# Kernel optimization log

Hardware: AMD Instinct MI355X
Metric: run time of the kernel (lower is better)

## Reference

```python
import jax, jax.numpy as jnp
import numpy as np

N = 8192
D = 256


def setup_inputs() -> dict:
    key = jax.random.key(0)
    ks = jax.random.split(key, 10)
    s = 1.0 / np.sqrt(D)
    inp = {
        "embeddings": jax.random.normal(ks[0], (N, D), dtype=jnp.float32),
        "adjacency": jax.random.randint(ks[1], (N, N), 0, 2, dtype=jnp.int32),
        "Wq": jax.random.uniform(ks[2], (D, D), jnp.float32, -s, s),
        "bq": jax.random.uniform(ks[3], (D,), jnp.float32, -s, s),
        "Wk": jax.random.uniform(ks[4], (D, D), jnp.float32, -s, s),
        "bk": jax.random.uniform(ks[5], (D,), jnp.float32, -s, s),
        "Wv": jax.random.uniform(ks[6], (D, D), jnp.float32, -s, s),
        "bv": jax.random.uniform(ks[7], (D,), jnp.float32, -s, s),
        "Wo": jax.random.uniform(ks[8], (D, D), jnp.float32, -s, s),
        "bo": jax.random.uniform(ks[9], (D,), jnp.float32, -s, s),
    }
    return inp


def reference(embeddings, adjacency, Wq, bq, Wk, bk, Wv, bv, Wo, bo):
    # Q/K/V projections (torch Linear: x @ W.T + b)
    Q = embeddings @ Wq.T + bq            # [N, D]
    K = embeddings @ Wk.T + bk            # [N, D]
    V = embeddings @ Wv.T + bv            # [N, D]
    scale = 1.0 / jnp.sqrt(jnp.asarray(D, dtype=embeddings.dtype))
    scores = (Q @ K.T) * scale            # [N, N]
    scores = jnp.where(adjacency == 0, jnp.asarray(-1e9, scores.dtype), scores)
    attn = jax.nn.softmax(scores, axis=-1)  # dropout is identity in eval mode
    context = attn @ V                    # [N, D]
    return context @ Wo.T + bo
```

## Files before the change

kernel.cpp:

```cpp
#include <hip/hip_runtime.h>
#include <hip/hip_bf16.h>


#define LOG2E 1.44269504088896340736f
#define MASKVAL -3.0e38f
#define MINIT   -1.0e38f

using f32x4 = __attribute__((ext_vector_type(4))) float;
using s16x8 = __attribute__((ext_vector_type(8))) short;
using s16x4 = __attribute__((ext_vector_type(4))) short;

__device__ __forceinline__ void gl_lds16(void* l, const void* g) {
  __builtin_amdgcn_global_load_lds(
      (const __attribute__((address_space(1))) void*)g,
      (__attribute__((address_space(3))) void*)l, 16, 0, 0);
}

__device__ __forceinline__ short f2bf(float x) {
  union { float f; unsigned u; } v; v.f = x;
  unsigned r = v.u + 0x7fffu + ((v.u >> 16) & 1u);
  return (short)(r >> 16);
}

__device__ __forceinline__ s16x8 cvt_frag(f32x4 a, f32x4 b) {
  s16x8 r;
  r[0]=f2bf(a[0]); r[1]=f2bf(a[1]); r[2]=f2bf(a[2]); r[3]=f2bf(a[3]);
  r[4]=f2bf(b[0]); r[5]=f2bf(b[1]); r[6]=f2bf(b[2]); r[7]=f2bf(b[3]);
  return r;
}

__device__ __forceinline__ f32x4 mfma16(s16x8 a, s16x8 b, f32x4 c) {
  return __builtin_amdgcn_mfma_f32_16x16x32_bf16(a, b, c, 0, 0, 0);
}

__global__ __launch_bounds__(256, 2)
void qkv_kernel(const float* __restrict__ E,
                const float* __restrict__ Wq, const float* __restrict__ bq,
                const float* __restrict__ Wk, const float* __restrict__ bk,
                const float* __restrict__ Wv, const float* __restrict__ bv,
                unsigned short* __restrict__ Qb, unsigned short* __restrict__ Kb,
                unsigned short* __restrict__ VT)
{
  const int tid = threadIdx.x, lane = tid & 63, w = tid >> 6;
  const int wr = w >> 1, wc = w & 1;
  const int l15 = lane & 15, lhi = lane >> 4;
  const int m0 = blockIdx.x * 64 + wr * 32;
  const int n0 = blockIdx.y * 64 + wc * 32;

  s16x8 af[2][8];
#pragma unroll
  for (int m = 0; m < 2; ++m) {
    const float* ap = E + (size_t)(m0 + m * 16 + l15) * 256 + lhi * 8;
#pragma unroll
    for (int ks = 0; ks < 8; ++ks) {
      f32x4 lo = *(const f32x4*)(ap + ks * 32);
      f32x4 hi = *(const f32x4*)(ap + ks * 32 + 4);
      af[m][ks] = cvt_frag(lo, hi);
    }
  }

  const float* Ws[3] = {Wq, Wk, Wv};
  f32x4 acc[3][2][2] = {};
#pragma unroll
  for (int mtx = 0; mtx < 3; ++mtx)
#pragma unroll
    for (int n = 0; n < 2; ++n) {
      const float* bp = Ws[mtx] + (size_t)(n0 + n * 16 + l15) * 256 + lhi * 8;
#pragma unroll
      for (int ks = 0; ks < 8; ++ks) {
        f32x4 lo = *(const f32x4*)(bp + ks * 32);
        f32x4 hi = *(const f32x4*)(bp + ks * 32 + 4);
        s16x8 bf = cvt_frag(lo, hi);
#pragma unroll
        for (int m = 0; m < 2; ++m)
          acc[mtx][m][n] = mfma16(af[m][ks], bf, acc[mtx][m][n]);
      }
    }

#pragma unroll
  for (int n = 0; n < 2; ++n) {
    int col = n0 + n * 16 + l15;
    float bvq = bq[col], bvk = bk[col], bvv = bv[col];
#pragma unroll
    for (int m = 0; m < 2; ++m) {
      int rbase = m0 + m * 16 + lhi * 4;
#pragma unroll
      for (int r = 0; r < 4; ++r) {
        Qb[(size_t)(rbase + r) * 256 + col] = (unsigned short)f2bf((acc[0][m][n][r] + bvq) * 0.0625f);
        Kb[(size_t)(rbase + r) * 256 + col] = (unsigned short)f2bf(acc[1][m][n][r] + bvk);
      }
      s16x4 pk;
#pragma unroll
      for (int r = 0; r < 4; ++r) pk[r] = f2bf(acc[2][m][n][r] + bvv);
      *(s16x4*)(VT + (size_t)col * 8192 + rbase) = pk;
    }
  }
}

__global__ __launch_bounds__(256, 2)
void projo_kernel(const unsigned short* __restrict__ CX, const float* __restrict__ Wo,
                  const float* __restrict__ bo, float* __restrict__ outp)
{
  const int tid = threadIdx.x, lane = tid & 63, w = tid >> 6;
  const int wr = w >> 1, wc = w & 1;
  const int l15 = lane & 15, lhi = lane >> 4;
  const int m0 = blockIdx.x * 64 + wr * 32;
  const int n0 = blockIdx.y * 64 + wc * 32;

  s16x8 af[2][8];
#pragma unroll
  for (int m = 0; m < 2; ++m) {
    const unsigned short* ap = CX + (size_t)(m0 + m * 16 + l15) * 256 + lhi * 8;
#pragma unroll
    for (int ks = 0; ks < 8; ++ks) af[m][ks] = *(const s16x8*)(ap + ks * 32);
  }

  f32x4 acc[2][2] = {};
#pragma unroll
  for (int n = 0; n < 2; ++n) {
    const float* bp = Wo + (size_t)(n0 + n * 16 + l15) * 256 + lhi * 8;
#pragma unroll
    for (int ks = 0; ks < 8; ++ks) {
      f32x4 lo = *(const f32x4*)(bp + ks * 32);
      f32x4 hi = *(const f32x4*)(bp + ks * 32 + 4);
      s16x8 bf = cvt_frag(lo, hi);
#pragma unroll
      for (int m = 0; m < 2; ++m)
        acc[m][n] = mfma16(af[m][ks], bf, acc[m][n]);
    }
  }

#pragma unroll
  for (int n = 0; n < 2; ++n) {
    int col = n0 + n * 16 + l15;
    float bv = bo[col];
#pragma unroll
    for (int m = 0; m < 2; ++m) {
      int rbase = m0 + m * 16 + lhi * 4;
#pragma unroll
      for (int r = 0; r < 4; ++r)
        outp[(size_t)(rbase + r) * 256 + col] = acc[m][n][r] + bv;
    }
  }
}

template<int SPLIT, bool DIRECT, bool PACC_BF16>
__global__ __launch_bounds__(512, 2)
void attn_kernel(const unsigned short* __restrict__ Qb, const char* __restrict__ Kb,
                 const char* __restrict__ VbT, const int* __restrict__ adj,
                 void* __restrict__ pacc, float* __restrict__ pm,
                 float* __restrict__ pl, unsigned short* __restrict__ CX)
{
  __shared__ __align__(16) char ldsK[2][16384];
  __shared__ __align__(16) char ldsV[2][16384];
  __shared__ __align__(16) char ldsP[8][2048];
  const int tid = threadIdx.x, lane = tid & 63, w = tid >> 6;
  const int l15 = lane & 15, lhi = lane >> 4;
  const int qt = blockIdx.x / SPLIT, sp = blockIdx.x % SPLIT;
  const int q0 = qt * 256 + w * 32;
  char* myP = ldsP[w];
  const int kv_begin = sp * (8192 / SPLIT);
  const int NT = 8192 / SPLIT / 32;

  s16x8 qf[2][8];
#pragma unroll
  for (int f = 0; f < 2; ++f) {
    const unsigned short* qp = Qb + (size_t)(q0 + f * 16 + l15) * 256 + lhi * 8;
#pragma unroll
    for (int ks = 0; ks < 8; ++ks) qf[f][ks] = *(const s16x8*)(qp + ks * 32);
  }

  f32x4 ctx[2][16] = {};
  float m_run[2][4], l_run[2][4];
#pragma unroll
  for (int f = 0; f < 2; ++f)
#pragma unroll
    for (int r = 0; r < 4; ++r) { m_run[f][r] = MINIT; l_run[f][r] = 0.f; }

  auto STAGE = [&](int buf, int tt) {
    const int kv0 = kv_begin + tt * 32;
    const char* kg = Kb + (size_t)kv0 * 512;
#pragma unroll
    for (int i = 0; i < 2; ++i) {
      int o = tid * 16 + i * 8192;
      int row = o >> 9, inrow = o & 511;
      gl_lds16(&ldsK[buf][o], kg + row * 512 + (inrow ^ ((row & 7) << 4)));
    }
#pragma unroll
    for (int i = 0; i < 2; ++i) {
      int o = tid * 16 + i * 8192;
      int row = o >> 6, inrow = o & 63;
      gl_lds16(&ldsV[buf][o], VbT + (size_t)row * 16384 + (size_t)kv0 * 2 + (inrow ^ ((row & 3) << 4)));
    }
  };

  STAGE(0, 0);
  __syncthreads();

  const int* abase = adj + (size_t)(q0 + (lane >> 5)) * 8192 + (lane & 31);

  for (int t = 0; t < NT; ++t) {
    const int cur = t & 1;
    const int kv0 = kv_begin + t * 32;

    int av[16];
    {
      const int* ap = abase + kv0;
#pragma unroll
      for (int j = 0; j < 16; ++j) av[j] = ap[(size_t)j * 2 * 8192];
    }
    if (t + 1 < NT) STAGE(cur ^ 1, t + 1);

    f32x4 sacc[2][2] = {};
    __builtin_amdgcn_s_setprio(1);
#pragma unroll
    for (int ks = 0; ks < 8; ++ks)
#pragma unroll
      for (int cg = 0; cg < 2; ++cg) {
        int row = cg * 16 + l15;
        s16x8 kf = *(const s16x8*)(&ldsK[cur][row * 512 + ((ks * 64 + lhi * 16) ^ ((row & 7) << 4))]);
        sacc[0][cg] = mfma16(qf[0][ks], kf, sacc[0][cg]);
        sacc[1][cg] = mfma16(qf[1][ks], kf, sacc[1][cg]);
      }
    __builtin_amdgcn_s_setprio(0);

    unsigned bmv[2][4] = {};
#pragma unroll
    for (int j = 0; j < 16; ++j) {
      unsigned long long b = __ballot(av[j] != 0);
      unsigned lo = (unsigned)b, hi = (unsigned)(b >> 32);
      const int row0 = 2 * j;
      const int f = row0 >> 4, g = (row0 >> 2) & 3, r = row0 & 3;
      bmv[f][r]     = (lhi == g) ? lo : bmv[f][r];
      bmv[f][r + 1] = (lhi == g) ? hi : bmv[f][r + 1];
    }

#pragma unroll
    for (int f = 0; f < 2; ++f)
#pragma unroll
      for (int r = 0; r < 4; ++r) {
        unsigned ms = bmv[f][r] >> l15;
#pragma unroll
        for (int cg = 0; cg < 2; ++cg)
          if (!((ms >> (cg * 16)) & 1u)) sacc[f][cg][r] = MASKVAL;
      }

    float tmax[2][4];
#pragma unroll
    for (int f = 0; f < 2; ++f)
#pragma unroll
      for (int r = 0; r < 4; ++r)
        tmax[f][r] = fmaxf(sacc[f][0][r], sacc[f][1][r]);
#pragma unroll
    for (int mk = 1; mk <= 8; mk <<= 1)
#pragma unroll
      for (int f = 0; f < 2; ++f)
#pragma unroll
        for (int r = 0; r < 4; ++r)
          tmax[f][r] = fmaxf(tmax[f][r], __shfl_xor(tmax[f][r], mk, 64));

    float need = MASKVAL;
#pragma unroll
    for (int f = 0; f < 2; ++f)
#pragma unroll
      for (int r = 0; r < 4; ++r)
        need = fmaxf(need, tmax[f][r] - m_run[f][r]);
    if (!__all(need <= 8.0f)) {
#pragma unroll
      for (int f = 0; f < 2; ++f) {
        f32x4 fv;
#pragma unroll
        for (int r = 0; r < 4; ++r) {
          float mnew = fmaxf(m_run[f][r], tmax[f][r]);
          float fs = __builtin_amdgcn_exp2f((m_run[f][r] - mnew) * LOG2E);
          m_run[f][r] = mnew; l_run[f][r] *= fs; fv[r] = fs;
        }
#pragma unroll
        for (int dm = 0; dm < 16; ++dm) ctx[f][dm] *= fv;
      }
    }

#pragma unroll
    for (int f = 0; f < 2; ++f)
#pragma unroll
      for (int cg = 0; cg < 2; ++cg)
#pragma unroll
        for (int r = 0; r < 4; ++r) {
          float p = __builtin_amdgcn_exp2f((sacc[f][cg][r] - m_run[f][r]) * LOG2E);
          l_run[f][r] += p;
          int row = f * 16 + lhi * 4 + r;
          int cb = (cg * 16 + l15) * 2;
          *(short*)(myP + row * 64 + (cb ^ ((row & 3) << 4))) = f2bf(p);
        }

    __builtin_amdgcn_s_setprio(1);
    s16x8 pf[2];
#pragma unroll
    for (int f = 0; f < 2; ++f) {
      int prow = f * 16 + l15;
      pf[f] = *(const s16x8*)(myP + prow * 64 + ((lhi * 16) ^ ((prow & 3) << 4)));
    }
#pragma unroll
    for (int dm = 0; dm < 16; ++dm) {
      int vrow = dm * 16 + l15;
      s16x8 vf = *(const s16x8*)(&ldsV[cur][vrow * 64 + ((lhi * 16) ^ ((vrow & 3) << 4))]);
      ctx[0][dm] = mfma16(pf[0], vf, ctx[0][dm]);
      ctx[1][dm] = mfma16(pf[1], vf, ctx[1][dm]);
    }
    __builtin_amdgcn_s_setprio(0);

    __syncthreads();
  }

#pragma unroll
  for (int mk = 1; mk <= 8; mk <<= 1)
#pragma unroll
    for (int f = 0; f < 2; ++f)
#pragma unroll
      for (int r = 0; r < 4; ++r)
        l_run[f][r] += __shfl_xor(l_run[f][r], mk, 64);

  if (DIRECT) {
#pragma unroll
    for (int f = 0; f < 2; ++f)
#pragma unroll
      for (int r = 0; r < 4; ++r) {
        float inv = 1.0f / l_run[f][r];
        size_t rowb = (size_t)(q0 + f * 16 + lhi * 4 + r) * 256 + l15;
#pragma unroll
        for (int dm = 0; dm < 16; ++dm)
          CX[rowb + dm * 16] = (unsigned short)f2bf(ctx[f][dm][r] * inv);
      }
  } else {
#pragma unroll
    for (int f = 0; f < 2; ++f)
#pragma unroll
      for (int r = 0; r < 4; ++r) {
        size_t rowb = (size_t)sp * 8192 * 256 +
                      (size_t)(q0 + f * 16 + lhi * 4 + r) * 256 + l15;
        if (PACC_BF16) {
#pragma unroll
          for (int dm = 0; dm < 16; ++dm)
            ((unsigned short*)pacc)[rowb + dm * 16] = (unsigned short)f2bf(ctx[f][dm][r]);
        } else {
#pragma unroll
          for (int dm = 0; dm < 16; ++dm)
            ((float*)pacc)[rowb + dm * 16] = ctx[f][dm][r];
        }
      }
    if (l15 == 0) {
#pragma unroll
      for (int f = 0; f < 2; ++f)
#pragma unroll
        for (int r = 0; r < 4; ++r) {
          pm[(size_t)sp * 8192 + q0 + f * 16 + lhi * 4 + r] = m_run[f][r];
          pl[(size_t)sp * 8192 + q0 + f * 16 + lhi * 4 + r] = l_run[f][r];
        }
    }
  }
}

template<bool PACC_BF16>
__global__ __launch_bounds__(256)
void combine_kernel(const void* __restrict__ pacc, const float* __restrict__ pm,
                    const float* __restrict__ pl, unsigned short* __restrict__ cx)
{
  const int row = blockIdx.x;
  const int d = threadIdx.x;
  float M = MINIT;
#pragma unroll
  for (int s = 0; s < 8; ++s) M = fmaxf(M, pm[s * 8192 + row]);
  float L = 0.f, v = 0.f;
#pragma unroll
  for (int s = 0; s < 8; ++s) {
    float ws = __builtin_amdgcn_exp2f((pm[s * 8192 + row] - M) * LOG2E);
    L += ws * pl[s * 8192 + row];
    size_t idx = (size_t)s * 8192 * 256 + (size_t)row * 256 + d;
    float pv;
    if (PACC_BF16) {
      union { unsigned u; float f; } c; c.u = (unsigned)((const unsigned short*)pacc)[idx] << 16;
      pv = c.f;
    } else {
      pv = ((const float*)pacc)[idx];
    }
    v += ws * pv;
  }
  cx[(size_t)row * 256 + d] = (unsigned short)f2bf(v / L);
}

extern "C" void kernel_launch(void* const* d_in, const int* in_sizes, int n_in,
                              void* d_out, int out_size, void* d_ws, size_t ws_size,
                              hipStream_t stream)
{
  const float* E  = (const float*)d_in[0];
  const int*  adj = (const int*)d_in[1];
  const float* Wq = (const float*)d_in[2];
  const float* bq = (const float*)d_in[3];
  const float* Wk = (const float*)d_in[4];
  const float* bk = (const float*)d_in[5];
  const float* Wv = (const float*)d_in[6];
  const float* bv = (const float*)d_in[7];
  const float* Wo = (const float*)d_in[8];
  const float* bo = (const float*)d_in[9];

  char* ws = (char*)d_ws;
  unsigned short* Qb = (unsigned short*)(ws);
  unsigned short* Kb = (unsigned short*)(ws + ((size_t)4 << 20));
  unsigned short* VT = (unsigned short*)(ws + ((size_t)8 << 20));
  unsigned short* CX = (unsigned short*)(ws + ((size_t)12 << 20));
  char* pacc = ws + ((size_t)16 << 20);

  hipLaunchKernelGGL(qkv_kernel, dim3(128, 4), dim3(256), 0, stream,
                     E, Wq, bq, Wk, bk, Wv, bv, Qb, Kb, VT);

  const size_t PACC_F32_BYTES  = (size_t)8 * 8192 * 256 * 4;
  const size_t PACC_BF16_BYTES = (size_t)8 * 8192 * 256 * 2;
  const size_t PMPL = (size_t)8 * 8192 * 4;
  const size_t NEED_F32  = ((size_t)16 << 20) + PACC_F32_BYTES + 2 * PMPL;
  const size_t NEED_BF16 = ((size_t)16 << 20) + PACC_BF16_BYTES + 2 * PMPL;

  if (ws_size >= NEED_F32) {
    float* pm = (float*)(pacc + PACC_F32_BYTES);
    float* pl = pm + 8 * 8192;
    hipLaunchKernelGGL((attn_kernel<8, false, false>), dim3(256), dim3(512), 0, stream,
                       Qb, (const char*)Kb, (const char*)VT, adj, pacc, pm, pl, CX);
    hipLaunchKernelGGL((combine_kernel<false>), dim3(8192), dim3(256), 0, stream, pacc, pm, pl, CX);
  } else if (ws_size >= NEED_BF16) {
    float* pm = (float*)(pacc + PACC_BF16_BYTES);
    float* pl = pm + 8 * 8192;
    hipLaunchKernelGGL((attn_kernel<8, false, true>), dim3(256), dim3(512), 0, stream,
                       Qb, (const char*)Kb, (const char*)VT, adj, pacc, pm, pl, CX);
    hipLaunchKernelGGL((combine_kernel<true>), dim3(8192), dim3(256), 0, stream, pacc, pm, pl, CX);
  } else {
    float* pm = (float*)pacc; float* pl = pm + 8192;
    hipLaunchKernelGGL((attn_kernel<1, true, false>), dim3(32), dim3(512), 0, stream,
                       Qb, (const char*)Kb, (const char*)VT, adj, pacc, pm, pl, CX);
  }
  hipLaunchKernelGGL(projo_kernel, dim3(128, 4), dim3(256), 0, stream, CX, Wo, bo, (float*)d_out);
}
```

Baseline: 618.5 us.

## Load K and V fragments directly from global memory instead of LDS staging

Removes the double-buffered LDS staging of K and V tiles and the per-tile block barrier, so each wave loads its MFMA operands straight from global memory (relying on L2/L1 caching). Blocks shrink from 8 waves to 4, with twice as many blocks launched. This drops barrier stalls and LDS traffic, but each wave now issues redundant global loads of the same K/V data, and the gathers are strided (especially V rows 16 KB apart), which adds latency and cache pressure.

After: 704.9 us. +14.0%, slower.

```diff
diff --git a/kernel.cpp b/kernel.cpp
--- a/kernel.cpp
+++ b/kernel.cpp
@@ -9,12 +9,6 @@
 using f32x4 = __attribute__((ext_vector_type(4))) float;
 using s16x8 = __attribute__((ext_vector_type(8))) short;
 using s16x4 = __attribute__((ext_vector_type(4))) short;
-
-__device__ __forceinline__ void gl_lds16(void* l, const void* g) {
-  __builtin_amdgcn_global_load_lds(
-      (const __attribute__((address_space(1))) void*)g,
-      (__attribute__((address_space(3))) void*)l, 16, 0, 0);
-}
 
 __device__ __forceinline__ short f2bf(float x) {
   union { float f; unsigned u; } v; v.f = x;
@@ -145,19 +139,18 @@
 }
 
 template<int SPLIT, bool DIRECT, bool PACC_BF16>
-__global__ __launch_bounds__(512, 2)
+__global__ __launch_bounds__(256, 2)
 void attn_kernel(const unsigned short* __restrict__ Qb, const char* __restrict__ Kb,
                  const char* __restrict__ VbT, const int* __restrict__ adj,
                  void* __restrict__ pacc, float* __restrict__ pm,
                  float* __restrict__ pl, unsigned short* __restrict__ CX)
 {
-  __shared__ __align__(16) char ldsK[2][16384];
-  __shared__ __align__(16) char ldsV[2][16384];
-  __shared__ __align__(16) char ldsP[8][2048];
+  __shared__ __align__(16) char ldsP[4][2048];
   const int tid = threadIdx.x, lane = tid & 63, w = tid >> 6;
   const int l15 = lane & 15, lhi = lane >> 4;
-  const int qt = blockIdx.x / SPLIT, sp = blockIdx.x % SPLIT;
-  const int q0 = qt * 256 + w * 32;
+  const int sp = blockIdx.x % SPLIT;
+  const int qt = (blockIdx.x / SPLIT) * 4 + w;
+  const int q0 = qt * 32;
   char* myP = ldsP[w];
   const int kv_begin = sp * (8192 / SPLIT);
   const int NT = 8192 / SPLIT / 32;
@@ -177,30 +170,11 @@
 #pragma unroll
     for (int r = 0; r < 4; ++r) { m_run[f][r] = MINIT; l_run[f][r] = 0.f; }
 
-  auto STAGE = [&](int buf, int tt) {
-    const int kv0 = kv_begin + tt * 32;
-    const char* kg = Kb + (size_t)kv0 * 512;
-#pragma unroll
-    for (int i = 0; i < 2; ++i) {
-      int o = tid * 16 + i * 8192;
-      int row = o >> 9, inrow = o & 511;
-      gl_lds16(&ldsK[buf][o], kg + row * 512 + (inrow ^ ((row & 7) << 4)));
-    }
-#pragma unroll
-    for (int i = 0; i < 2; ++i) {
-      int o = tid * 16 + i * 8192;
-      int row = o >> 6, inrow = o & 63;
-      gl_lds16(&ldsV[buf][o], VbT + (size_t)row * 16384 + (size_t)kv0 * 2 + (inrow ^ ((row & 3) << 4)));
-    }
-  };
-
-  STAGE(0, 0);
-  __syncthreads();
-
   const int* abase = adj + (size_t)(q0 + (lane >> 5)) * 8192 + (lane & 31);
+  const char* kbase0 = Kb + (size_t)l15 * 512 + lhi * 16;
+  const char* vbase0 = VbT + (size_t)l15 * 16384 + lhi * 16;
 
   for (int t = 0; t < NT; ++t) {
-    const int cur = t & 1;
     const int kv0 = kv_begin + t * 32;
 
     int av[16];
@@ -209,19 +183,19 @@
 #pragma unroll
       for (int j = 0; j < 16; ++j) av[j] = ap[(size_t)j * 2 * 8192];
     }
-    if (t + 1 < NT) STAGE(cur ^ 1, t + 1);
 
     f32x4 sacc[2][2] = {};
+    const char* kb = kbase0 + (size_t)kv0 * 512;
     __builtin_amdgcn_s_setprio(1);
 #pragma unroll
-    for (int ks = 0; ks < 8; ++ks)
-#pragma unroll
-      for (int cg = 0; cg < 2; ++cg) {
-        int row = cg * 16 + l15;
-        s16x8 kf = *(const s16x8*)(&ldsK[cur][row * 512 + ((ks * 64 + lhi * 16) ^ ((row & 7) << 4))]);
-        sacc[0][cg] = mfma16(qf[0][ks], kf, sacc[0][cg]);
-        sacc[1][cg] = mfma16(qf[1][ks], kf, sacc[1][cg]);
-      }
+    for (int ks = 0; ks < 8; ++ks) {
+      s16x8 kf0 = *(const s16x8*)(kb + ks * 64);
+      s16x8 kf1 = *(const s16x8*)(kb + 16 * 512 + ks * 64);
+      sacc[0][0] = mfma16(qf[0][ks], kf0, sacc[0][0]);
+      sacc[1][0] = mfma16(qf[1][ks], kf0, sacc[1][0]);
+      sacc[0][1] = mfma16(qf[0][ks], kf1, sacc[0][1]);
+      sacc[1][1] = mfma16(qf[1][ks], kf1, sacc[1][1]);
+    }
     __builtin_amdgcn_s_setprio(0);
 
     unsigned bmv[2][4] = {};
@@ -293,23 +267,21 @@
           *(short*)(myP + row * 64 + (cb ^ ((row & 3) << 4))) = f2bf(p);
         }
 
-    __builtin_amdgcn_s_setprio(1);
     s16x8 pf[2];
 #pragma unroll
     for (int f = 0; f < 2; ++f) {
       int prow = f * 16 + l15;
       pf[f] = *(const s16x8*)(myP + prow * 64 + ((lhi * 16) ^ ((prow & 3) << 4)));
     }
+    const char* vb = vbase0 + (size_t)kv0 * 2;
+    __builtin_amdgcn_s_setprio(1);
 #pragma unroll
     for (int dm = 0; dm < 16; ++dm) {
-      int vrow = dm * 16 + l15;
-      s16x8 vf = *(const s16x8*)(&ldsV[cur][vrow * 64 + ((lhi * 16) ^ ((vrow & 3) << 4))]);
+      s16x8 vf = *(const s16x8*)(vb + (size_t)dm * 16 * 16384);
       ctx[0][dm] = mfma16(pf[0], vf, ctx[0][dm]);
       ctx[1][dm] = mfma16(pf[1], vf, ctx[1][dm]);
     }
     __builtin_amdgcn_s_setprio(0);
-
-    __syncthreads();
   }
 
 #pragma unroll
@@ -422,18 +394,18 @@
   if (ws_size >= NEED_F32) {
     float* pm = (float*)(pacc + PACC_F32_BYTES);
     float* pl = pm + 8 * 8192;
-    hipLaunchKernelGGL((attn_kernel<8, false, false>), dim3(256), dim3(512), 0, stream,
+    hipLaunchKernelGGL((attn_kernel<8, false, false>), dim3(512), dim3(256), 0, stream,
                        Qb, (const char*)Kb, (const char*)VT, adj, pacc, pm, pl, CX);
     hipLaunchKernelGGL((combine_kernel<false>), dim3(8192), dim3(256), 0, stream, pacc, pm, pl, CX);
   } else if (ws_size >= NEED_BF16) {
     float* pm = (float*)(pacc + PACC_BF16_BYTES);
     float* pl = pm + 8 * 8192;
-    hipLaunchKernelGGL((attn_kernel<8, false, true>), dim3(256), dim3(512), 0, stream,
+    hipLaunchKernelGGL((attn_kernel<8, false, true>), dim3(512), dim3(256), 0, stream,
                        Qb, (const char*)Kb, (const char*)VT, adj, pacc, pm, pl, CX);
     hipLaunchKernelGGL((combine_kernel<true>), dim3(8192), dim3(256), 0, stream, pacc, pm, pl, CX);
   } else {
     float* pm = (float*)pacc; float* pl = pm + 8192;
-    hipLaunchKernelGGL((attn_kernel<1, true, false>), dim3(32), dim3(512), 0, stream,
+    hipLaunchKernelGGL((attn_kernel<1, true, false>), dim3(64), dim3(256), 0, stream,
                        Qb, (const char*)Kb, (const char*)VT, adj, pacc, pm, pl, CX);
   }
   hipLaunchKernelGGL(projo_kernel, dim3(128, 4), dim3(256), 0, stream, CX, Wo, bo, (float*)d_out);
```
